# Performance work log

Hardware: AMD Instinct MI355X
Metric: run time of the kernel (lower is better)

## Reference

```python
import jax, jax.numpy as jnp
import numpy as np

N_NODES = 50000
N_EDGES = 1_600_000
IN_DIM = 128
HID = 32
HEADS = 4
NEG_SLOPE = 0.2


def setup_inputs() -> dict:
    key = jax.random.key(0)
    ks = jax.random.split(key, 6)
    h = jax.random.normal(ks[0], (N_NODES, IN_DIM), dtype=jnp.float32)
    src = jax.random.randint(ks[1], (N_EDGES,), 0, N_NODES, dtype=jnp.int32)
    dst = jax.random.randint(ks[2], (N_EDGES,), 0, N_NODES, dtype=jnp.int32)
    s = 1.0 / np.sqrt(IN_DIM)  # ~ Linear default init scale
    Wq = (jax.random.normal(ks[3], (HEADS, IN_DIM, HID), dtype=jnp.float32) * s)
    Wk = (jax.random.normal(ks[4], (HEADS, IN_DIM, HID), dtype=jnp.float32) * s)
    Wv = (jax.random.normal(ks[5], (HEADS, IN_DIM, HID), dtype=jnp.float32) * s)
    return {"h": h, "src": src, "dst": dst, "Wq": Wq, "Wk": Wk, "Wv": Wv}


def _gat_forward(h, src, dst, Wq, Wk, Wv):
    n = h.shape[0]
    # per-head projections: [H, N, D]
    q = jnp.einsum('ni,hio->hno', h, Wq)
    k = jnp.einsum('ni,hio->hno', h, Wk)
    v = jnp.einsum('ni,hio->hno', h, Wv)
    # edge scores: e = leaky_relu(<q_src, k_dst>)  -> [H, E]
    e = jax.nn.leaky_relu(jnp.einsum('hed,hed->he', q[:, src], k[:, dst]),
                          negative_slope=NEG_SLOPE)
    # segment softmax over incoming edges of each dst node
    seg_max = jax.vmap(lambda x: jax.ops.segment_max(x, dst, num_segments=n))(e)
    seg_max = jax.lax.stop_gradient(jnp.where(jnp.isfinite(seg_max), seg_max, 0.0))
    ex = jnp.exp(e - seg_max[:, dst])                       # [H, E]
    denom = jax.vmap(lambda x: jax.ops.segment_sum(x, dst, num_segments=n))(ex)
    alpha = ex / jnp.maximum(denom, 1e-9)[:, dst]           # [H, E]
    # weighted scatter-sum of source values into dst nodes: [H, N, D]
    msg = alpha[..., None] * v[:, src]
    out = jax.vmap(lambda m: jax.ops.segment_sum(m, dst, num_segments=n))(msg)
    # concat heads along feature dim -> [N, H*D]
    return out.transpose(1, 0, 2).reshape(n, HEADS * HID)


def reference(h, src, dst, Wq, Wk, Wv):
    return _gat_forward(h, src, dst, Wq, Wk, Wv)
```

## Files before the change

### kernel.cpp

```cpp
#include <hip/hip_runtime.h>
#include <hip/hip_fp16.h>

#define IN_DIM 128
#define HID 32
#define HEADS 4
#define OUTC (HEADS*HID)
#define NEG_SLOPE 0.2f
#define PAD 96
#define BSHIFT 7
#define BNODES 128
#define BCAP 6144
#define MAXBUCK 512
#define NCOLS 384

typedef _Float16 f16x8 __attribute__((ext_vector_type(8)));
typedef float    f32x4 __attribute__((ext_vector_type(4)));

__device__ __forceinline__ unsigned short f2h(float f) {
    return __half_as_ushort(__float2half_rn(f));
}
__device__ __forceinline__ float2 h2f2(unsigned u) {
    __half2 h = *reinterpret_cast<__half2*>(&u);
    return __half22float2(h);
}
__device__ __forceinline__ float qdot(const uint4& qv, const float4& kd) {
    float2 a = h2f2(qv.x);
    float2 b = h2f2(qv.y);
    return a.x * kd.x + a.y * kd.y + b.x * kd.z + b.y * kd.w;
}
__device__ __forceinline__ void vacc(const uint4& qv, float e, float4& acc) {
    float2 a = h2f2(qv.z);
    float2 b = h2f2(qv.w);
    acc.x = fmaf(e, a.x, acc.x);
    acc.y = fmaf(e, a.y, acc.y);
    acc.z = fmaf(e, b.x, acc.z);
    acc.w = fmaf(e, b.y, acc.w);
}

__global__ __launch_bounds__(256) void w_prep(
    const float* __restrict__ Wq, const float* __restrict__ Wk,
    const float* __restrict__ Wv, unsigned short* __restrict__ Wt)
{
    int idx = blockIdx.x * 256 + threadIdx.x;
    if (idx >= NCOLS * IN_DIM) return;
    int c = idx >> 7, k = idx & 127;
    int sel = c >> 7;
    int cc  = c & 127;
    int head = cc >> 5, dcol = cc & 31;
    const float* W = (sel == 0) ? Wk : (sel == 1) ? Wq : Wv;
    Wt[idx] = f2h(W[(size_t)head * IN_DIM * HID + (size_t)k * HID + dcol]);
}

__global__ __launch_bounds__(256) void gat_proj_mfma(
    const float* __restrict__ h, const unsigned short* __restrict__ Wt,
    float* __restrict__ Ko, unsigned short* __restrict__ QV, int n)
{
    __shared__ unsigned short hsm[32 * IN_DIM];
    const int tid  = threadIdx.x;
    const int row0 = blockIdx.x * 32;

    for (int idx = tid; idx < 32 * 64; idx += 256) {
        int r  = idx >> 6;
        int c2 = idx & 63;
        int gr = row0 + r;
        float2 hv = (gr < n) ? ((const float2*)h)[(size_t)gr * 64 + c2]
                             : make_float2(0.f, 0.f);
        int col = c2 * 2;
        int sc  = col ^ ((r & 7) << 3);
        __half2 packed = __floats2half2_rn(hv.x, hv.y);
        *(unsigned*)&hsm[r * IN_DIM + sc] = *(unsigned*)&packed;
    }
    __syncthreads();

    const int w = tid >> 6;
    const int l = tid & 63;
    const int l15 = l & 15;
    const int kg  = l >> 4;
    const _Float16* Wt16 = (const _Float16*)Wt;

    f32x4 acc[2][6];
#pragma unroll
    for (int rt = 0; rt < 2; ++rt)
#pragma unroll
        for (int ct = 0; ct < 6; ++ct) acc[rt][ct] = (f32x4){0.f, 0.f, 0.f, 0.f};

#pragma unroll
    for (int s = 0; s < 4; ++s) {
        int scol = (s * 32 + kg * 8) ^ ((l & 7) << 3);
        f16x8 a0 = *(const f16x8*)&hsm[l15 * IN_DIM + scol];
        f16x8 a1 = *(const f16x8*)&hsm[(l15 + 16) * IN_DIM + scol];
#pragma unroll
        for (int ct = 0; ct < 6; ++ct) {
            int c = w * 96 + ct * 16 + l15;
            f16x8 b = *(const f16x8*)&Wt16[(size_t)c * IN_DIM + s * 32 + kg * 8];
            acc[0][ct] = __builtin_amdgcn_mfma_f32_16x16x32_f16(a0, b, acc[0][ct], 0, 0, 0);
            acc[1][ct] = __builtin_amdgcn_mfma_f32_16x16x32_f16(a1, b, acc[1][ct], 0, 0, 0);
        }
    }

#pragma unroll
    for (int rt = 0; rt < 2; ++rt) {
#pragma unroll
        for (int ct = 0; ct < 6; ++ct) {
            int cD = w * 96 + ct * 16 + l15;
#pragma unroll
            for (int r = 0; r < 4; ++r) {
                int node = row0 + rt * 16 + kg * 4 + r;
                if (node >= n) continue;
                float v = acc[rt][ct][r];
                if (cD < 128) {
                    Ko[(size_t)node * OUTC + cD] = v;
                } else if (cD < 256) {
                    int cq = cD - 128;
                    QV[(size_t)node * 256 + (cq >> 2) * 8 + (cq & 3)] = f2h(v);
                } else {
                    int cv = cD - 256;
                    QV[(size_t)node * 256 + (cv >> 2) * 8 + (cv & 3) + 4] = f2h(v);
                }
            }
        }
    }
}

__global__ __launch_bounds__(256) void gat_bin(
    const int* __restrict__ src, const int* __restrict__ dst,
    int* __restrict__ gcount, unsigned* __restrict__ pairs,
    int ne, int nbuck)
{
    __shared__ int hist[MAXBUCK];
    __shared__ int base[MAXBUCK];
    const int tid = threadIdx.x;
    for (int i = tid; i < nbuck; i += 256) hist[i] = 0;
    __syncthreads();

    const int ne4 = ne >> 2;
    const int4* s4 = (const int4*)src;
    const int4* d4 = (const int4*)dst;

    int4 sv[4], dv[4];
    int loc[16], bk[16];
    bool val[4];
#pragma unroll
    for (int k = 0; k < 4; ++k) {
        int idx = blockIdx.x * 1024 + k * 256 + tid;
        val[k] = idx < ne4;
        if (val[k]) { sv[k] = s4[idx]; dv[k] = d4[idx]; }
        else { sv[k] = make_int4(0,0,0,0); dv[k] = make_int4(0,0,0,0); }
    }
#pragma unroll
    for (int k = 0; k < 4; ++k) {
        int dd[4] = { dv[k].x, dv[k].y, dv[k].z, dv[k].w };
#pragma unroll
        for (int j = 0; j < 4; ++j) {
            int b = dd[j] >> BSHIFT;
            bk[k*4+j]  = b;
            loc[k*4+j] = val[k] ? atomicAdd(&hist[b], 1) : 0;
        }
    }
    __syncthreads();
    for (int i = tid; i < nbuck; i += 256)
        base[i] = hist[i] ? atomicAdd(&gcount[i], hist[i]) : 0;
    __syncthreads();
#pragma unroll
    for (int k = 0; k < 4; ++k) {
        if (!val[k]) continue;
        int ss[4] = { sv[k].x, sv[k].y, sv[k].z, sv[k].w };
        int dd[4] = { dv[k].x, dv[k].y, dv[k].z, dv[k].w };
#pragma unroll
        for (int j = 0; j < 4; ++j) {
            int b = bk[k*4+j];
            int p = base[b] + loc[k*4+j];
            if (p < BCAP)
                pairs[(size_t)b * BCAP + p] =
                    ((unsigned)ss[j] << BSHIFT) | (unsigned)(dd[j] & (BNODES-1));
        }
    }
    if (blockIdx.x == 0 && tid == 0) {
        for (int e = ne4 * 4; e < ne; ++e) {
            int b = dst[e] >> BSHIFT;
            int p = atomicAdd(&gcount[b], 1);
            if (p < BCAP)
                pairs[(size_t)b * BCAP + p] =
                    ((unsigned)src[e] << BSHIFT) | (unsigned)(dst[e] & (BNODES-1));
        }
    }
}

#define SBINS 128
__global__ __launch_bounds__(256) void gat_bscatter(
    const unsigned* __restrict__ pairs, const int* __restrict__ gcount,
    int* __restrict__ cnt, int* __restrict__ slots, int n)
{
    __shared__ unsigned buf[BCAP];
    __shared__ unsigned sorted[BCAP];
    __shared__ int cl[BNODES];
    __shared__ int bh[SBINS], bb[SBINS], bc[SBINS];
    const int b   = blockIdx.x;
    const int tid = threadIdx.x;
    if (tid < BNODES) cl[tid] = 0;
    if (tid < SBINS) bh[tid] = 0;
    __syncthreads();

    int m = gcount[b];
    if (m > BCAP) m = BCAP;
    const unsigned* pb = pairs + (size_t)b * BCAP;

    for (int i = tid; i < m; i += 256) {
        unsigned p = pb[i];
        buf[i] = p;
        atomicAdd(&bh[(p >> BSHIFT) >> 9], 1);
    }
    __syncthreads();

    if (tid < SBINS) bb[tid] = bh[tid];
    __syncthreads();
    for (int off = 1; off < SBINS; off <<= 1) {
        int v = 0;
        if (tid < SBINS && tid >= off) v = bb[tid - off];
        __syncthreads();
        if (tid < SBINS) bb[tid] += v;
        __syncthreads();
    }
    if (tid < SBINS) { bb[tid] -= bh[tid]; bc[tid] = bb[tid]; }
    __syncthreads();

    for (int i = tid; i < m; i += 256) {
        unsigned p = buf[i];
        int pos = atomicAdd(&bc[(p >> BSHIFT) >> 9], 1);
        sorted[pos] = p;
    }
    __syncthreads();

    for (int i = tid; i < m; i += 256) {
        unsigned p = sorted[i];
        int dl  = p & (BNODES - 1);
        int s   = p >> BSHIFT;
        int pos = atomicAdd(&cl[dl], 1);
        if (pos < PAD) slots[((size_t)b * BNODES + dl) * PAD + pos] = s;
    }
    __syncthreads();
    int node = b * BNODES + tid;
    if (tid < BNODES && node < n) cnt[node] = cl[tid];
}

__global__ __launch_bounds__(256) void gat_gather(
    const int* __restrict__ slots, const int* __restrict__ cnt,
    const uint4* __restrict__ QV, const float4* __restrict__ K4,
    float* __restrict__ out, int n)
{
    int wid = (blockIdx.x * blockDim.x + threadIdx.x) >> 6;
    if (wid >= n) return;
    const int lane = threadIdx.x & 63;
    const int l32  = lane & 31;
    const int g    = lane >> 5;

    const float4 kd = K4[(size_t)wid * 32 + l32];

    int deg = cnt[wid];
    if (deg > PAD) deg = PAD;
    const int* row = slots + (size_t)wid * PAD;

    const int half0 = (deg + 1) >> 1;
    const int jb = g ? half0 : 0;
    const int je = g ? deg   : half0;

    float4 acc = make_float4(0.f, 0.f, 0.f, 0.f);
    float  dsum = 0.f;

    int j = jb;
    for (; j + 3 < je; j += 4) {
        int s0 = row[j], s1 = row[j + 1], s2 = row[j + 2], s3 = row[j + 3];
        uint4 w0 = QV[(size_t)s0 * 32 + l32];
        uint4 w1 = QV[(size_t)s1 * 32 + l32];
        uint4 w2 = QV[(size_t)s2 * 32 + l32];
        uint4 w3 = QV[(size_t)s3 * 32 + l32];

        float p0 = qdot(w0, kd), p1 = qdot(w1, kd);
        float p2 = qdot(w2, kd), p3 = qdot(w3, kd);
#pragma unroll
        for (int off = 1; off < 8; off <<= 1) {
            p0 += __shfl_xor(p0, off, 8);
            p1 += __shfl_xor(p1, off, 8);
            p2 += __shfl_xor(p2, off, 8);
            p3 += __shfl_xor(p3, off, 8);
        }
        float e0 = __expf(p0 > 0.f ? p0 : NEG_SLOPE * p0);
        float e1 = __expf(p1 > 0.f ? p1 : NEG_SLOPE * p1);
        float e2 = __expf(p2 > 0.f ? p2 : NEG_SLOPE * p2);
        float e3 = __expf(p3 > 0.f ? p3 : NEG_SLOPE * p3);
        dsum += (e0 + e1) + (e2 + e3);
        vacc(w0, e0, acc); vacc(w1, e1, acc);
        vacc(w2, e2, acc); vacc(w3, e3, acc);
    }
    for (; j < je; ++j) {
        int s0 = row[j];
        uint4 w0 = QV[(size_t)s0 * 32 + l32];
        float p0 = qdot(w0, kd);
#pragma unroll
        for (int off = 1; off < 8; off <<= 1) p0 += __shfl_xor(p0, off, 8);
        float e0 = __expf(p0 > 0.f ? p0 : NEG_SLOPE * p0);
        dsum += e0;
        vacc(w0, e0, acc);
    }

    acc.x += __shfl_xor(acc.x, 32, 64);
    acc.y += __shfl_xor(acc.y, 32, 64);
    acc.z += __shfl_xor(acc.z, 32, 64);
    acc.w += __shfl_xor(acc.w, 32, 64);
    dsum  += __shfl_xor(dsum, 32, 64);

    if (g == 0) {
        float inv = 1.f / fmaxf(dsum, 1e-9f);
        float4 o; o.x = acc.x*inv; o.y = acc.y*inv; o.z = acc.z*inv; o.w = acc.w*inv;
        ((float4*)out)[(size_t)wid * 32 + l32] = o;
    }
}

extern "C" void kernel_launch(void* const* d_in, const int* in_sizes, int n_in,
                              void* d_out, int out_size, void* d_ws, size_t ws_size,
                              hipStream_t stream) {
    const float* h   = (const float*)d_in[0];
    const int*   src = (const int*)d_in[1];
    const int*   dst = (const int*)d_in[2];
    const float* Wq  = (const float*)d_in[3];
    const float* Wk  = (const float*)d_in[4];
    const float* Wv  = (const float*)d_in[5];
    float* out = (float*)d_out;

    const int n     = in_sizes[0] / IN_DIM;
    const int ne    = in_sizes[1];
    const int nbuck = (n + BNODES - 1) >> BSHIFT;

    float*          K      = (float*)d_ws;
    unsigned short* QV     = (unsigned short*)(K + (size_t)n * OUTC);
    int*            cnt    = (int*)(QV + (size_t)n * 256);
    int*            slots  = cnt + n;
    int*            gcount = slots + (size_t)n * PAD;
    unsigned*       pairs  = (unsigned*)(gcount + MAXBUCK);
    unsigned short* Wt     = (unsigned short*)(pairs + (size_t)MAXBUCK * BCAP);

    hipMemsetAsync(gcount, 0, MAXBUCK * sizeof(int), stream);

    w_prep<<<(NCOLS * IN_DIM + 255) / 256, 256, 0, stream>>>(Wq, Wk, Wv, Wt);
    gat_proj_mfma<<<(n + 31) / 32, 256, 0, stream>>>(h, Wt, K, QV, n);

    int ne4 = ne >> 2;
    int binblk = (ne4 + 1023) / 1024;
    gat_bin<<<binblk, 256, 0, stream>>>(src, dst, gcount, pairs, ne, nbuck);
    gat_bscatter<<<nbuck, 256, 0, stream>>>(pairs, gcount, cnt, slots, n);

    int gblk = (n * 64 + 255) / 256;
    gat_gather<<<gblk, 256, 0, stream>>>(slots, cnt, (const uint4*)QV,
                                         (const float4*)K, out, n);
}
```

Measured before the change: 188.0 us.

## Fuse bucket scatter and gather into one kernel with per-subbucket shared CSR

Replaces the separate scatter kernel, which wrote padded per-node slot lists to global memory, and the gather kernel with a single kernel. Each block handles a 16-node sub-range of a 128-node bucket. It counts and scatters source ids into a shared-memory CSR, then runs the attention aggregation directly from shared memory. This removes the global slots/cnt round trip and one launch, and the memset is folded into w_prep. In exchange, each bucket's pair list is read eight times (once per sub-block), source ids are stored as 16-bit and so assume fewer than 65536 nodes, and the per-node degree cap of 96 is replaced by a 1024 cap per sub-block.

```diff
diff --git a/kernel.cpp b/kernel.cpp
--- a/kernel.cpp
+++ b/kernel.cpp
@@ -6,12 +6,13 @@
 #define HEADS 4
 #define OUTC (HEADS*HID)
 #define NEG_SLOPE 0.2f
-#define PAD 96
 #define BSHIFT 7
 #define BNODES 128
 #define BCAP 6144
 #define MAXBUCK 512
 #define NCOLS 384
+#define SUBN 16
+#define SCAP 1024
 
 typedef _Float16 f16x8 __attribute__((ext_vector_type(8)));
 typedef float    f32x4 __attribute__((ext_vector_type(4)));
@@ -39,9 +40,11 @@
 
 __global__ __launch_bounds__(256) void w_prep(
     const float* __restrict__ Wq, const float* __restrict__ Wk,
-    const float* __restrict__ Wv, unsigned short* __restrict__ Wt)
+    const float* __restrict__ Wv, unsigned short* __restrict__ Wt,
+    int* __restrict__ gcount)
 {
     int idx = blockIdx.x * 256 + threadIdx.x;
+    if (idx < MAXBUCK) gcount[idx] = 0;
     if (idx >= NCOLS * IN_DIM) return;
     int c = idx >> 7, k = idx & 127;
     int sel = c >> 7;
@@ -186,133 +189,116 @@
     }
 }
 
-#define SBINS 128
-__global__ __launch_bounds__(256) void gat_bscatter(
+__global__ __launch_bounds__(256) void gat_bucket(
     const unsigned* __restrict__ pairs, const int* __restrict__ gcount,
-    int* __restrict__ cnt, int* __restrict__ slots, int n)
+    const uint4* __restrict__ QV, const float4* __restrict__ K4,
+    float* __restrict__ out, int n, int nbuck)
 {
-    __shared__ unsigned buf[BCAP];
-    __shared__ unsigned sorted[BCAP];
-    __shared__ int cl[BNODES];
-    __shared__ int bh[SBINS], bb[SBINS], bc[SBINS];
-    const int b   = blockIdx.x;
+    __shared__ unsigned short sl[SCAP];
+    __shared__ int cl[SUBN], cur[SUBN], off[SUBN + 1];
+
+    const int blk = blockIdx.x;
+    const int sub = (blk >> 3) & 7;
+    const int b   = (blk >> 6) * 8 + (blk & 7);
+    if (b >= nbuck) return;
     const int tid = threadIdx.x;
-    if (tid < BNODES) cl[tid] = 0;
-    if (tid < SBINS) bh[tid] = 0;
-    __syncthreads();
-
-    int m = gcount[b];
-    if (m > BCAP) m = BCAP;
+
+    if (tid < SUBN) cl[tid] = 0;
+    __syncthreads();
+
+    int m = gcount[b]; if (m > BCAP) m = BCAP;
     const unsigned* pb = pairs + (size_t)b * BCAP;
 
+    for (int i = tid; i < m; i += 256) {
+        int dl = pb[i] & (BNODES - 1);
+        if ((dl >> 4) == sub) atomicAdd(&cl[dl & (SUBN - 1)], 1);
+    }
+    __syncthreads();
+    if (tid == 0) {
+        int acc = 0;
+#pragma unroll
+        for (int i = 0; i < SUBN; ++i) { off[i] = acc; cur[i] = acc; acc += cl[i]; }
+        off[SUBN] = acc;
+    }
+    __syncthreads();
     for (int i = tid; i < m; i += 256) {
         unsigned p = pb[i];
-        buf[i] = p;
-        atomicAdd(&bh[(p >> BSHIFT) >> 9], 1);
-    }
-    __syncthreads();
-
-    if (tid < SBINS) bb[tid] = bh[tid];
-    __syncthreads();
-    for (int off = 1; off < SBINS; off <<= 1) {
-        int v = 0;
-        if (tid < SBINS && tid >= off) v = bb[tid - off];
-        __syncthreads();
-        if (tid < SBINS) bb[tid] += v;
-        __syncthreads();
-    }
-    if (tid < SBINS) { bb[tid] -= bh[tid]; bc[tid] = bb[tid]; }
-    __syncthreads();
-
-    for (int i = tid; i < m; i += 256) {
-        unsigned p = buf[i];
-        int pos = atomicAdd(&bc[(p >> BSHIFT) >> 9], 1);
-        sorted[pos] = p;
-    }
-    __syncthreads();
-
-    for (int i = tid; i < m; i += 256) {
-        unsigned p = sorted[i];
-        int dl  = p & (BNODES - 1);
-        int s   = p >> BSHIFT;
-        int pos = atomicAdd(&cl[dl], 1);
-        if (pos < PAD) slots[((size_t)b * BNODES + dl) * PAD + pos] = s;
-    }
-    __syncthreads();
-    int node = b * BNODES + tid;
-    if (tid < BNODES && node < n) cnt[node] = cl[tid];
-}
-
-__global__ __launch_bounds__(256) void gat_gather(
-    const int* __restrict__ slots, const int* __restrict__ cnt,
-    const uint4* __restrict__ QV, const float4* __restrict__ K4,
-    float* __restrict__ out, int n)
-{
-    int wid = (blockIdx.x * blockDim.x + threadIdx.x) >> 6;
-    if (wid >= n) return;
-    const int lane = threadIdx.x & 63;
+        int dl = p & (BNODES - 1);
+        if ((dl >> 4) == sub) {
+            int pos = atomicAdd(&cur[dl & (SUBN - 1)], 1);
+            if (pos < SCAP) sl[pos] = (unsigned short)(p >> BSHIFT);
+        }
+    }
+    __syncthreads();
+
+    const int w    = tid >> 6;
+    const int lane = tid & 63;
     const int l32  = lane & 31;
     const int g    = lane >> 5;
 
-    const float4 kd = K4[(size_t)wid * 32 + l32];
-
-    int deg = cnt[wid];
-    if (deg > PAD) deg = PAD;
-    const int* row = slots + (size_t)wid * PAD;
-
-    const int half0 = (deg + 1) >> 1;
-    const int jb = g ? half0 : 0;
-    const int je = g ? deg   : half0;
-
-    float4 acc = make_float4(0.f, 0.f, 0.f, 0.f);
-    float  dsum = 0.f;
-
-    int j = jb;
-    for (; j + 3 < je; j += 4) {
-        int s0 = row[j], s1 = row[j + 1], s2 = row[j + 2], s3 = row[j + 3];
-        uint4 w0 = QV[(size_t)s0 * 32 + l32];
-        uint4 w1 = QV[(size_t)s1 * 32 + l32];
-        uint4 w2 = QV[(size_t)s2 * 32 + l32];
-        uint4 w3 = QV[(size_t)s3 * 32 + l32];
-
-        float p0 = qdot(w0, kd), p1 = qdot(w1, kd);
-        float p2 = qdot(w2, kd), p3 = qdot(w3, kd);
-#pragma unroll
-        for (int off = 1; off < 8; off <<= 1) {
-            p0 += __shfl_xor(p0, off, 8);
-            p1 += __shfl_xor(p1, off, 8);
-            p2 += __shfl_xor(p2, off, 8);
-            p3 += __shfl_xor(p3, off, 8);
-        }
-        float e0 = __expf(p0 > 0.f ? p0 : NEG_SLOPE * p0);
-        float e1 = __expf(p1 > 0.f ? p1 : NEG_SLOPE * p1);
-        float e2 = __expf(p2 > 0.f ? p2 : NEG_SLOPE * p2);
-        float e3 = __expf(p3 > 0.f ? p3 : NEG_SLOPE * p3);
-        dsum += (e0 + e1) + (e2 + e3);
-        vacc(w0, e0, acc); vacc(w1, e1, acc);
-        vacc(w2, e2, acc); vacc(w3, e3, acc);
-    }
-    for (; j < je; ++j) {
-        int s0 = row[j];
-        uint4 w0 = QV[(size_t)s0 * 32 + l32];
-        float p0 = qdot(w0, kd);
-#pragma unroll
-        for (int off = 1; off < 8; off <<= 1) p0 += __shfl_xor(p0, off, 8);
-        float e0 = __expf(p0 > 0.f ? p0 : NEG_SLOPE * p0);
-        dsum += e0;
-        vacc(w0, e0, acc);
-    }
-
-    acc.x += __shfl_xor(acc.x, 32, 64);
-    acc.y += __shfl_xor(acc.y, 32, 64);
-    acc.z += __shfl_xor(acc.z, 32, 64);
-    acc.w += __shfl_xor(acc.w, 32, 64);
-    dsum  += __shfl_xor(dsum, 32, 64);
-
-    if (g == 0) {
-        float inv = 1.f / fmaxf(dsum, 1e-9f);
-        float4 o; o.x = acc.x*inv; o.y = acc.y*inv; o.z = acc.z*inv; o.w = acc.w*inv;
-        ((float4*)out)[(size_t)wid * 32 + l32] = o;
+#pragma unroll
+    for (int q = 0; q < SUBN / 4; ++q) {
+        int nl   = q * 4 + w;
+        int node = b * BNODES + sub * SUBN + nl;
+        if (node >= n) continue;
+
+        const int e0  = off[nl];
+        const int deg = off[nl + 1] - e0;
+        const float4 kd = K4[(size_t)node * 32 + l32];
+
+        float4 acc = make_float4(0.f, 0.f, 0.f, 0.f);
+        float  dsum = 0.f;
+
+        const int half0 = (deg + 1) >> 1;
+        int j  = e0 + (g ? half0 : 0);
+        const int je = e0 + (g ? deg : half0);
+
+        for (; j + 3 < je; j += 4) {
+            int s0 = sl[j], s1 = sl[j + 1], s2 = sl[j + 2], s3 = sl[j + 3];
+            uint4 w0 = QV[(size_t)s0 * 32 + l32];
+            uint4 w1 = QV[(size_t)s1 * 32 + l32];
+            uint4 w2 = QV[(size_t)s2 * 32 + l32];
+            uint4 w3 = QV[(size_t)s3 * 32 + l32];
+
+            float p0 = qdot(w0, kd), p1 = qdot(w1, kd);
+            float p2 = qdot(w2, kd), p3 = qdot(w3, kd);
+#pragma unroll
+            for (int off2 = 1; off2 < 8; off2 <<= 1) {
+                p0 += __shfl_xor(p0, off2, 8);
+                p1 += __shfl_xor(p1, off2, 8);
+                p2 += __shfl_xor(p2, off2, 8);
+                p3 += __shfl_xor(p3, off2, 8);
+            }
+            float e0f = __expf(p0 > 0.f ? p0 : NEG_SLOPE * p0);
+            float e1f = __expf(p1 > 0.f ? p1 : NEG_SLOPE * p1);
+            float e2f = __expf(p2 > 0.f ? p2 : NEG_SLOPE * p2);
+            float e3f = __expf(p3 > 0.f ? p3 : NEG_SLOPE * p3);
+            dsum += (e0f + e1f) + (e2f + e3f);
+            vacc(w0, e0f, acc); vacc(w1, e1f, acc);
+            vacc(w2, e2f, acc); vacc(w3, e3f, acc);
+        }
+        for (; j < je; ++j) {
+            int s0 = sl[j];
+            uint4 w0 = QV[(size_t)s0 * 32 + l32];
+            float p0 = qdot(w0, kd);
+#pragma unroll
+            for (int off2 = 1; off2 < 8; off2 <<= 1) p0 += __shfl_xor(p0, off2, 8);
+            float e0f = __expf(p0 > 0.f ? p0 : NEG_SLOPE * p0);
+            dsum += e0f;
+            vacc(w0, e0f, acc);
+        }
+
+        acc.x += __shfl_xor(acc.x, 32, 64);
+        acc.y += __shfl_xor(acc.y, 32, 64);
+        acc.z += __shfl_xor(acc.z, 32, 64);
+        acc.w += __shfl_xor(acc.w, 32, 64);
+        dsum  += __shfl_xor(dsum, 32, 64);
+
+        if (g == 0) {
+            float inv = 1.f / fmaxf(dsum, 1e-9f);
+            float4 o; o.x = acc.x*inv; o.y = acc.y*inv; o.z = acc.z*inv; o.w = acc.w*inv;
+            ((float4*)out)[(size_t)node * 32 + l32] = o;
+        }
     }
 }
 
@@ -333,23 +319,18 @@
 
     float*          K      = (float*)d_ws;
     unsigned short* QV     = (unsigned short*)(K + (size_t)n * OUTC);
-    int*            cnt    = (int*)(QV + (size_t)n * 256);
-    int*            slots  = cnt + n;
-    int*            gcount = slots + (size_t)n * PAD;
+    int*            gcount = (int*)(QV + (size_t)n * 256);
     unsigned*       pairs  = (unsigned*)(gcount + MAXBUCK);
     unsigned short* Wt     = (unsigned short*)(pairs + (size_t)MAXBUCK * BCAP);
 
-    hipMemsetAsync(gcount, 0, MAXBUCK * sizeof(int), stream);
-
-    w_prep<<<(NCOLS * IN_DIM + 255) / 256, 256, 0, stream>>>(Wq, Wk, Wv, Wt);
+    w_prep<<<(NCOLS * IN_DIM + 255) / 256, 256, 0, stream>>>(Wq, Wk, Wv, Wt, gcount);
     gat_proj_mfma<<<(n + 31) / 32, 256, 0, stream>>>(h, Wt, K, QV, n);
 
     int ne4 = ne >> 2;
     int binblk = (ne4 + 1023) / 1024;
     gat_bin<<<binblk, 256, 0, stream>>>(src, dst, gcount, pairs, ne, nbuck);
-    gat_bscatter<<<nbuck, 256, 0, stream>>>(pairs, gcount, cnt, slots, n);
-
-    int gblk = (n * 64 + 255) / 256;
-    gat_gather<<<gblk, 256, 0, stream>>>(slots, cnt, (const uint4*)QV,
-                                         (const float4*)K, out, n);
-}
+
+    int nb8  = (nbuck + 7) / 8;
+    gat_bucket<<<nb8 * 64, 256, 0, stream>>>(pairs, gcount, (const uint4*)QV,
+                                             (const float4*)K, out, n, nbuck);
+}
```

Result: faster. 183.7 us (-2.3%).
